# Performance work log

Hardware: AMD Instinct MI355X
Metric: run time of the kernel (lower is better)

The kernel has to match this reference:

```python
import jax, jax.numpy as jnp
import numpy as np

N_NODES = 50000
N_NEIB = 64
D = 256
BATCH = 1024
N_SAMPLES = (25, 10)  # fanout per layer (layer_specs n_sample)


def setup_inputs() -> dict:
    key = jax.random.key(0)
    ks = jax.random.split(key, 12)
    inp = {
        'ids': jax.random.randint(ks[0], (BATCH,), 0, N_NODES),
        'diff_idx': jax.random.randint(ks[1], (N_NODES, N_NEIB), 0, N_NODES),
        'diff_val': jax.random.uniform(ks[2], (N_NODES, N_NEIB), dtype=jnp.float32),
        'feats': jax.random.normal(ks[3], (N_NODES, D), dtype=jnp.float32),
    }
    # two aggregator layers, each: fc_x, fc_neib : D -> D (= output_dim//2)
    for li in range(2):
        inp[f'Wx{li+1}'] = jax.random.normal(ks[4 + 4 * li], (D, D), dtype=jnp.float32) * 0.05
        inp[f'bx{li+1}'] = jnp.zeros((D,), dtype=jnp.float32)
        inp[f'Wn{li+1}'] = jax.random.normal(ks[5 + 4 * li], (D, D), dtype=jnp.float32) * 0.05
        inp[f'bn{li+1}'] = jnp.zeros((D,), dtype=jnp.float32)
    return inp


def _sample(diff_idx, diff_val, ids, n_samples, key):
    # gather candidate neighbor rows, shared random column permutation, take first n_samples
    tmp_idx = diff_idx[ids]            # [n, N_NEIB]
    tmp_val = diff_val[ids]
    perm = jax.random.permutation(key, tmp_idx.shape[1])
    idx = tmp_idx[:, perm][:, :n_samples].reshape(-1)
    val = tmp_val[:, perm][:, :n_samples].reshape(-1)
    return idx, val


def _agg(x, neib, vals, Wx, bx, Wn, bn):
    # weighted-mean neighbor aggregation + self/neib linear combine + relu
    n = x.shape[0]
    d = neib.shape[1]
    neib = neib.reshape(n, -1, d)              # [n, s, d]
    vals = vals.reshape(n, -1)                 # [n, s]
    w = vals / (jnp.sum(vals, axis=1, keepdims=True) + 1e-10)
    m = jnp.einsum('nsd,ns->nd', neib, w)      # weighted mean of neighbors
    return jax.nn.relu(x @ Wx + bx + m @ Wn + bn)


def reference(ids, diff_idx, diff_val, feats,
              Wx1, bx1, Wn1, bn1, Wx2, bx2, Wn2, bn2):
    skey = jax.random.key(42)
    all_feats = [feats[ids]]
    all_vals = []
    cur = ids
    for li, n in enumerate(N_SAMPLES):
        cur, vals = _sample(diff_idx, diff_val, cur, n, jax.random.fold_in(skey, li))
        all_feats.append(feats[cur])
        all_vals.append(vals)
    params = [(Wx1, bx1, Wn1, bn1), (Wx2, bx2, Wn2, bn2)]
    for Wx, bx, Wn, bn in params:
        all_feats = [_agg(all_feats[k], all_feats[k + 1], all_vals[k], Wx, bx, Wn, bn)
                     for k in range(len(all_feats) - 1)]
    assert len(all_feats) == 1
    return all_feats[0]  # [BATCH, D]
```

## Files before the change

### kernel.cpp

```cpp
#include <hip/hip_runtime.h>
#include <stdint.h>
#include <stddef.h>
#include <algorithm>

#define BATCH  1024
#define S1     25
#define S2     10
#define DIM    256
#define NNEIB  64
#define L2ROWS (BATCH * S1)
#define MROWS  (BATCH + BATCH * S1)
#define KTOT   512
#define NFEAT  50000

struct Perm25 { int p[S1]; };
struct Perm10 { int p[S2]; };

typedef __attribute__((ext_vector_type(8))) short short8;
typedef __attribute__((ext_vector_type(4))) float f32x4;

static inline uint32_t rotl_(uint32_t x, int d) { return (x << d) | (x >> (32 - d)); }

static void tf2x32(uint32_t k0, uint32_t k1, uint32_t x0, uint32_t x1,
                   uint32_t* o0, uint32_t* o1) {
  const uint32_t ks0 = k0, ks1 = k1, ks2 = k0 ^ k1 ^ 0x1BD11BDAu;
  static const int R[8] = {13, 15, 26, 6, 17, 29, 16, 24};
  x0 += ks0; x1 += ks1;
  for (int g = 0; g < 5; ++g) {
    const int* rr = R + (g & 1) * 4;
    for (int i = 0; i < 4; i++) { x0 += x1; x1 = rotl_(x1, rr[i]); x1 ^= x0; }
    uint32_t a, b;
    switch (g) {
      default:
      case 0: a = ks1; b = ks2; break;
      case 1: a = ks2; b = ks0; break;
      case 2: a = ks0; b = ks1; break;
      case 3: a = ks1; b = ks2; break;
      case 4: a = ks2; b = ks0; break;
    }
    x0 += a; x1 = x1 + b + (uint32_t)(g + 1);
  }
  *o0 = x0; *o1 = x1;
}

static void compute_perm(uint32_t li, int n, int* out) {
  uint32_t k0, k1, s0, s1;
  tf2x32(0u, 42u, 0u, li, &k0, &k1);
  tf2x32(k0, k1, 0u, 1u, &s0, &s1);
  uint32_t bits[NNEIB];
  for (int i = 0; i < NNEIB; i++) {
    uint32_t a, b;
    tf2x32(s0, s1, 0u, (uint32_t)i, &a, &b);
    bits[i] = a ^ b;
  }
  int idx[NNEIB];
  for (int i = 0; i < NNEIB; i++) idx[i] = i;
  std::stable_sort(idx, idx + NNEIB, [&](int A, int B) { return bits[A] < bits[B]; });
  for (int j = 0; j < n; j++) out[j] = idx[j];
}

__device__ __forceinline__ unsigned short f2bf(float x) {
  union { float f; uint32_t u; } v; v.f = x;
  uint32_t r = (v.u + 0x7FFFu + ((v.u >> 16) & 1u)) >> 16;
  return (unsigned short)r;
}
__device__ __forceinline__ float bfbits2f(uint32_t lo16) {
  union { uint32_t u; float f; } v; v.u = lo16 << 16;
  return v.f;
}
__device__ __forceinline__ void gload16(const unsigned short* g, unsigned short* l) {
  __builtin_amdgcn_global_load_lds(
      (const __attribute__((address_space(1))) unsigned int*)g,
      (__attribute__((address_space(3))) unsigned int*)l, 16, 0, 0);
}


#define PREP_CONVF   12500
#define PREP_CONVW   512
#define PREP_BLOCKS  (PREP_CONVF + 2 * PREP_CONVW + 4)
__global__ __launch_bounds__(256) void prep_k(
    const float* __restrict__ feats, uint32_t* __restrict__ fb,
    const float* __restrict__ Wx1, const float* __restrict__ Wn1,
    unsigned short* __restrict__ Wt1,
    const float* __restrict__ Wx2, const float* __restrict__ Wn2,
    unsigned short* __restrict__ Wt2,
    const int* __restrict__ ids, const int* __restrict__ dix,
    const float* __restrict__ dval, int* __restrict__ idx1,
    float* __restrict__ w1, Perm25 pm) {
  int b = blockIdx.x, t = threadIdx.x;
  if (b < PREP_CONVF) {
    int i = b * 256 + t;
    f32x4 v = *(const f32x4*)&feats[(size_t)i * 4];
    uint2 o;
    o.x = f2bf(v.x) | ((uint32_t)f2bf(v.y) << 16);
    o.y = f2bf(v.z) | ((uint32_t)f2bf(v.w) << 16);
    ((uint2*)fb)[i] = o;
  } else if (b < PREP_CONVF + 2 * PREP_CONVW) {
    int wi = b - PREP_CONVF;
    const float* Wx = (wi < PREP_CONVW) ? Wx1 : Wx2;
    const float* Wn = (wi < PREP_CONVW) ? Wn1 : Wn2;
    unsigned short* Wt = (wi < PREP_CONVW) ? Wt1 : Wt2;
    int idx = (wi % PREP_CONVW) * 256 + t;
    int n = idx >> 9, k = idx & 511;
    float v = (k < DIM) ? Wx[(size_t)k * DIM + n] : Wn[(size_t)(k - DIM) * DIM + n];
    Wt[(size_t)n * KTOT + k] = f2bf(v);
  } else {
    int i = (b - PREP_CONVF - 2 * PREP_CONVW) * 256 + t;
    if (i >= BATCH) return;
    int nid = ids[i];
    const float* vr = dval + (size_t)nid * NNEIB;
    const int* ir = dix + (size_t)nid * NNEIB;
    float v[S1];
    float s = 0.f;
    for (int j = 0; j < S1; j++) { v[j] = vr[pm.p[j]]; s += v[j]; }
    float inv = 1.f / (s + 1e-10f);
    for (int j = 0; j < S1; j++) {
      w1[i * S1 + j] = v[j] * inv;
      idx1[i * S1 + j] = ir[pm.p[j]];
    }
  }
}

__global__ __launch_bounds__(256) void stage1_k(
    const uint2* __restrict__ fb, const int* __restrict__ ids,
    const int* __restrict__ idx1, const float* __restrict__ w1,
    const int* __restrict__ dix, const float* __restrict__ dval, Perm10 pm2,
    uint2* __restrict__ A1) {
  int wave = threadIdx.x >> 6, lane = threadIdx.x & 63;
  int r = blockIdx.x * 4 + wave;
  float a0 = 0.f, a1 = 0.f, a2 = 0.f, a3 = 0.f;
  int xr;
  if (r < BATCH) {
    xr = ids[r];
    int nbl = 0; float wl = 0.f;
    if (lane < S1) { nbl = idx1[r * S1 + lane]; wl = w1[r * S1 + lane]; }
#pragma unroll
    for (int j = 0; j < S1; j++) {
      int nid = __shfl(nbl, j);
      float wj = __shfl(wl, j);
      uint2 u = fb[(size_t)nid * 64 + lane];
      a0 += wj * bfbits2f(u.x & 0xffffu);
      a1 += wj * bfbits2f(u.x >> 16);
      a2 += wj * bfbits2f(u.y & 0xffffu);
      a3 += wj * bfbits2f(u.y >> 16);
    }
  } else {
    int nx = idx1[r - BATCH];
    xr = nx;
    int nbl = 0; float vj = 0.f;
    if (lane < S2) {
      int c = pm2.p[lane];
      nbl = dix[(size_t)nx * NNEIB + c];
      vj = dval[(size_t)nx * NNEIB + c];
    }
    float tot = 0.f;
#pragma unroll
    for (int j = 0; j < S2; j++) tot += __shfl(vj, j);
    float wl = vj / (tot + 1e-10f);
#pragma unroll
    for (int j = 0; j < S2; j++) {
      int nid = __shfl(nbl, j);
      float wj = __shfl(wl, j);
      uint2 u = fb[(size_t)nid * 64 + lane];
      a0 += wj * bfbits2f(u.x & 0xffffu);
      a1 += wj * bfbits2f(u.x >> 16);
      a2 += wj * bfbits2f(u.y & 0xffffu);
      a3 += wj * bfbits2f(u.y >> 16);
    }
  }
  uint2 xv = fb[(size_t)xr * 64 + lane];
  uint2 o;
  o.x = f2bf(a0) | ((uint32_t)f2bf(a1) << 16);
  o.y = f2bf(a2) | ((uint32_t)f2bf(a3) << 16);
  A1[(size_t)r * 128 + lane] = xv;
  A1[(size_t)r * 128 + 64 + lane] = o;
}

__global__ __launch_bounds__(256) void stage2_k(
    const uint2* __restrict__ Hb, const float* __restrict__ w1,
    uint2* __restrict__ A2) {
  int wave = threadIdx.x >> 6, lane = threadIdx.x & 63;
  int i = blockIdx.x * 4 + wave;
  float wl = (lane < S1) ? w1[(size_t)i * S1 + lane] : 0.f;
  const uint2* hb = Hb + (size_t)(BATCH + i * S1) * 64 + lane;
  float a0 = 0.f, a1 = 0.f, a2 = 0.f, a3 = 0.f;
#pragma unroll
  for (int j = 0; j < S1; j++) {
    float wj = __shfl(wl, j);
    uint2 u = hb[(size_t)j * 64];
    a0 += wj * bfbits2f(u.x & 0xffffu);
    a1 += wj * bfbits2f(u.x >> 16);
    a2 += wj * bfbits2f(u.y & 0xffffu);
    a3 += wj * bfbits2f(u.y >> 16);
  }
  uint2 xv = Hb[(size_t)i * 64 + lane];
  uint2 o;
  o.x = f2bf(a0) | ((uint32_t)f2bf(a1) << 16);
  o.y = f2bf(a2) | ((uint32_t)f2bf(a3) << 16);
  A2[(size_t)i * 128 + lane] = xv;
  A2[(size_t)i * 128 + 64 + lane] = o;
}

#define BK 32
template <int TBM, int TBN, bool OUT_BF16>
__global__ __launch_bounds__(256) void gemm_k(
    const unsigned short* __restrict__ A, const unsigned short* __restrict__ Wt,
    const float* __restrict__ bx, const float* __restrict__ bn,
    void* __restrict__ OutP) {
  constexpr int MI = TBM / 32;
  constexpr int NJ = TBN / 32;
  __shared__ __align__(16) unsigned short As[TBM][BK];
  __shared__ __align__(16) unsigned short Bs[TBN][BK];
  int t = threadIdx.x;
  int wave = t >> 6, lane = t & 63, quad = lane >> 4, l16 = lane & 15;
  int wm = (wave >> 1) * (TBM / 2);
  int wn = (wave & 1) * (TBN / 2);
  int row0 = blockIdx.x * TBM, col0 = blockIdx.y * TBN;

  f32x4 acc[MI][NJ];
#pragma unroll
  for (int i = 0; i < MI; i++)
#pragma unroll
    for (int j = 0; j < NJ; j++) acc[i][j] = (f32x4){0.f, 0.f, 0.f, 0.f};

  int rl = lane >> 2;
  int cl = (lane & 3) * 8;

  for (int k0 = 0; k0 < KTOT; k0 += BK) {
#pragma unroll
    for (int c = 0; c < TBM / 64; c++) {
      int row = c * 64 + wave * 16 + rl;
      gload16(A + (size_t)(row0 + row) * KTOT + k0 + cl, &As[c * 64 + wave * 16][0]);
    }
#pragma unroll
    for (int c = 0; c < TBN / 64; c++) {
      int row = c * 64 + wave * 16 + rl;
      gload16(Wt + (size_t)(col0 + row) * KTOT + k0 + cl, &Bs[c * 64 + wave * 16][0]);
    }
    __syncthreads();

    short8 af[MI], bfr[NJ];
#pragma unroll
    for (int i = 0; i < MI; i++)
      af[i] = *(const short8*)&As[wm + i * 16 + l16][quad * 8];
#pragma unroll
    for (int j = 0; j < NJ; j++)
      bfr[j] = *(const short8*)&Bs[wn + j * 16 + l16][quad * 8];
#pragma unroll
    for (int i = 0; i < MI; i++)
#pragma unroll
      for (int j = 0; j < NJ; j++)
        acc[i][j] = __builtin_amdgcn_mfma_f32_16x16x32_bf16(af[i], bfr[j], acc[i][j], 0, 0, 0);
    __syncthreads();
  }

  float bias[NJ];
#pragma unroll
  for (int j = 0; j < NJ; j++) {
    int c = col0 + wn + j * 16 + l16;
    bias[j] = bx[c] + bn[c];
  }
#pragma unroll
  for (int i = 0; i < MI; i++) {
#pragma unroll
    for (int j = 0; j < NJ; j++) {
      int c = col0 + wn + j * 16 + l16;
#pragma unroll
      for (int reg = 0; reg < 4; reg++) {
        int r = row0 + wm + i * 16 + quad * 4 + reg;
        float v = fmaxf(acc[i][j][reg] + bias[j], 0.f);
        if (OUT_BF16)
          ((unsigned short*)OutP)[(size_t)r * DIM + c] = f2bf(v);
        else
          ((float*)OutP)[(size_t)r * DIM + c] = v;
      }
    }
  }
}

static inline size_t align256(size_t x) { return (x + 255) & ~(size_t)255; }

extern "C" void kernel_launch(void* const* d_in, const int* in_sizes, int n_in,
                              void* d_out, int out_size, void* d_ws, size_t ws_size,
                              hipStream_t stream) {
  const int*   ids  = (const int*)d_in[0];
  const int*   dix  = (const int*)d_in[1];
  const float* dval = (const float*)d_in[2];
  const float* feats= (const float*)d_in[3];
  const float* Wx1  = (const float*)d_in[4];
  const float* bx1  = (const float*)d_in[5];
  const float* Wn1  = (const float*)d_in[6];
  const float* bn1  = (const float*)d_in[7];
  const float* Wx2  = (const float*)d_in[8];
  const float* bx2  = (const float*)d_in[9];
  const float* Wn2  = (const float*)d_in[10];
  const float* bn2  = (const float*)d_in[11];
  float* out = (float*)d_out;

  Perm25 p25;
  Perm10 p10;
  compute_perm(0u, S1, p25.p);
  compute_perm(1u, S2, p10.p);

  char* w = (char*)d_ws;
  int*            idx1 = (int*)w;            w += align256(sizeof(int) * L2ROWS);
  float*          w1   = (float*)w;          w += align256(sizeof(float) * L2ROWS);
  uint32_t*       fb   = (uint32_t*)w;       w += align256(2 * (size_t)NFEAT * DIM);
  unsigned short* A1   = (unsigned short*)w; w += align256(2 * (size_t)MROWS * KTOT);
  unsigned short* Hb   = (unsigned short*)w; w += align256(2 * (size_t)MROWS * DIM);
  unsigned short* A2   = (unsigned short*)w; w += align256(2 * (size_t)BATCH * KTOT);
  unsigned short* Wt1  = (unsigned short*)w; w += align256(2 * (size_t)DIM * KTOT);
  unsigned short* Wt2  = (unsigned short*)w; w += align256(2 * (size_t)DIM * KTOT);

  prep_k<<<PREP_BLOCKS, 256, 0, stream>>>(feats, fb, Wx1, Wn1, Wt1, Wx2, Wn2, Wt2,
                                          ids, dix, dval, idx1, w1, p25);
  stage1_k<<<MROWS / 4, 256, 0, stream>>>((const uint2*)fb, ids, idx1, w1, dix, dval,
                                          p10, (uint2*)A1);
  gemm_k<128, 128, true><<<dim3(MROWS / 128, DIM / 128), 256, 0, stream>>>(
      A1, Wt1, bx1, bn1, Hb);
  stage2_k<<<BATCH / 4, 256, 0, stream>>>((const uint2*)Hb, w1, (uint2*)A2);
  gemm_k<64, 64, false><<<dim3(BATCH / 64, DIM / 64), 256, 0, stream>>>(
      A2, Wt2, bx2, bn2, out);
}
```

Baseline: 182.9 us.

## Gather self features directly in GEMM and aggregate neighbor pairs with 16-byte loads

The stage kernels no longer copy self-feature rows into a concatenated A buffer. The GEMM instead gathers x rows straight from the bf16 feature table (via ids/idx1) for the first half of K and reads the separate aggregated-neighbor buffer for the second half. Stage1 also splits each wave into two 32-lane halves that each fetch a full 512-byte row with uint4 loads, handling two neighbors per iteration, then combines the halves with a cross-lane shuffle. This removes a write and reread of the self-feature half and halves the gather loop trip count, at the cost of scattered row reads inside the GEMM A-tile loads.

```diff
diff --git a/kernel.cpp b/kernel.cpp
--- a/kernel.cpp
+++ b/kernel.cpp
@@ -121,32 +121,36 @@
   }
 }
 
+template <int S>
+__device__ __forceinline__ void agg_pairs(const uint4* __restrict__ fb, int nbl,
+                                          float wl, int lane, float a[8]) {
+  int h = lane >> 5, l5 = lane & 31;
+#pragma unroll
+  for (int p = 0; p < (S + 1) / 2; p++) {
+    int jj = 2 * p + h;
+    int nid = __shfl(nbl, (jj < S) ? jj : 0);
+    float wj = (jj < S) ? __shfl(wl, jj) : 0.f;
+    uint4 u = fb[(size_t)nid * 32 + l5];
+    a[0] += wj * bfbits2f(u.x & 0xffffu); a[1] += wj * bfbits2f(u.x >> 16);
+    a[2] += wj * bfbits2f(u.y & 0xffffu); a[3] += wj * bfbits2f(u.y >> 16);
+    a[4] += wj * bfbits2f(u.z & 0xffffu); a[5] += wj * bfbits2f(u.z >> 16);
+    a[6] += wj * bfbits2f(u.w & 0xffffu); a[7] += wj * bfbits2f(u.w >> 16);
+  }
+}
+
 __global__ __launch_bounds__(256) void stage1_k(
-    const uint2* __restrict__ fb, const int* __restrict__ ids,
-    const int* __restrict__ idx1, const float* __restrict__ w1,
-    const int* __restrict__ dix, const float* __restrict__ dval, Perm10 pm2,
-    uint2* __restrict__ A1) {
+    const uint4* __restrict__ fb, const int* __restrict__ idx1,
+    const float* __restrict__ w1, const int* __restrict__ dix,
+    const float* __restrict__ dval, Perm10 pm2, uint4* __restrict__ M1) {
   int wave = threadIdx.x >> 6, lane = threadIdx.x & 63;
   int r = blockIdx.x * 4 + wave;
-  float a0 = 0.f, a1 = 0.f, a2 = 0.f, a3 = 0.f;
-  int xr;
+  float a[8] = {0.f, 0.f, 0.f, 0.f, 0.f, 0.f, 0.f, 0.f};
   if (r < BATCH) {
-    xr = ids[r];
     int nbl = 0; float wl = 0.f;
     if (lane < S1) { nbl = idx1[r * S1 + lane]; wl = w1[r * S1 + lane]; }
-#pragma unroll
-    for (int j = 0; j < S1; j++) {
-      int nid = __shfl(nbl, j);
-      float wj = __shfl(wl, j);
-      uint2 u = fb[(size_t)nid * 64 + lane];
-      a0 += wj * bfbits2f(u.x & 0xffffu);
-      a1 += wj * bfbits2f(u.x >> 16);
-      a2 += wj * bfbits2f(u.y & 0xffffu);
-      a3 += wj * bfbits2f(u.y >> 16);
-    }
+    agg_pairs<S1>(fb, nbl, wl, lane, a);
   } else {
     int nx = idx1[r - BATCH];
-    xr = nx;
     int nbl = 0; float vj = 0.f;
     if (lane < S2) {
       int c = pm2.p[lane];
@@ -157,28 +161,23 @@
 #pragma unroll
     for (int j = 0; j < S2; j++) tot += __shfl(vj, j);
     float wl = vj / (tot + 1e-10f);
-#pragma unroll
-    for (int j = 0; j < S2; j++) {
-      int nid = __shfl(nbl, j);
-      float wj = __shfl(wl, j);
-      uint2 u = fb[(size_t)nid * 64 + lane];
-      a0 += wj * bfbits2f(u.x & 0xffffu);
-      a1 += wj * bfbits2f(u.x >> 16);
-      a2 += wj * bfbits2f(u.y & 0xffffu);
-      a3 += wj * bfbits2f(u.y >> 16);
-    }
-  }
-  uint2 xv = fb[(size_t)xr * 64 + lane];
-  uint2 o;
-  o.x = f2bf(a0) | ((uint32_t)f2bf(a1) << 16);
-  o.y = f2bf(a2) | ((uint32_t)f2bf(a3) << 16);
-  A1[(size_t)r * 128 + lane] = xv;
-  A1[(size_t)r * 128 + 64 + lane] = o;
+    agg_pairs<S2>(fb, nbl, wl, lane, a);
+  }
+#pragma unroll
+  for (int q = 0; q < 8; q++) a[q] += __shfl_xor(a[q], 32);
+  if (lane < 32) {
+    uint4 o;
+    o.x = f2bf(a[0]) | ((uint32_t)f2bf(a[1]) << 16);
+    o.y = f2bf(a[2]) | ((uint32_t)f2bf(a[3]) << 16);
+    o.z = f2bf(a[4]) | ((uint32_t)f2bf(a[5]) << 16);
+    o.w = f2bf(a[6]) | ((uint32_t)f2bf(a[7]) << 16);
+    M1[(size_t)r * 32 + (lane & 31)] = o;
+  }
 }
 
 __global__ __launch_bounds__(256) void stage2_k(
     const uint2* __restrict__ Hb, const float* __restrict__ w1,
-    uint2* __restrict__ A2) {
+    uint2* __restrict__ M2) {
   int wave = threadIdx.x >> 6, lane = threadIdx.x & 63;
   int i = blockIdx.x * 4 + wave;
   float wl = (lane < S1) ? w1[(size_t)i * S1 + lane] : 0.f;
@@ -193,20 +192,19 @@
     a2 += wj * bfbits2f(u.y & 0xffffu);
     a3 += wj * bfbits2f(u.y >> 16);
   }
-  uint2 xv = Hb[(size_t)i * 64 + lane];
   uint2 o;
   o.x = f2bf(a0) | ((uint32_t)f2bf(a1) << 16);
   o.y = f2bf(a2) | ((uint32_t)f2bf(a3) << 16);
-  A2[(size_t)i * 128 + lane] = xv;
-  A2[(size_t)i * 128 + 64 + lane] = o;
+  M2[(size_t)i * 64 + lane] = o;
 }
 
 #define BK 32
-template <int TBM, int TBN, bool OUT_BF16>
+template <int TBM, int TBN, bool OUT_BF16, bool GATHER>
 __global__ __launch_bounds__(256) void gemm_k(
-    const unsigned short* __restrict__ A, const unsigned short* __restrict__ Wt,
-    const float* __restrict__ bx, const float* __restrict__ bn,
-    void* __restrict__ OutP) {
+    const unsigned short* __restrict__ Ax, const int* __restrict__ ids,
+    const int* __restrict__ idx1, const unsigned short* __restrict__ Am,
+    const unsigned short* __restrict__ Wt, const float* __restrict__ bx,
+    const float* __restrict__ bn, void* __restrict__ OutP) {
   constexpr int MI = TBM / 32;
   constexpr int NJ = TBN / 32;
   __shared__ __align__(16) unsigned short As[TBM][BK];
@@ -226,12 +224,20 @@
   int rl = lane >> 2;
   int cl = (lane & 3) * 8;
 
+  const unsigned short* xsrc[TBM / 64];
+  const unsigned short* msrc[TBM / 64];
+#pragma unroll
+  for (int c = 0; c < TBM / 64; c++) {
+    int grow = row0 + c * 64 + wave * 16 + rl;
+    int xr = GATHER ? ((grow < BATCH) ? ids[grow] : idx1[grow - BATCH]) : grow;
+    xsrc[c] = Ax + (size_t)xr * DIM + cl;
+    msrc[c] = Am + (size_t)grow * DIM + cl - DIM;
+  }
+
   for (int k0 = 0; k0 < KTOT; k0 += BK) {
 #pragma unroll
-    for (int c = 0; c < TBM / 64; c++) {
-      int row = c * 64 + wave * 16 + rl;
-      gload16(A + (size_t)(row0 + row) * KTOT + k0 + cl, &As[c * 64 + wave * 16][0]);
-    }
+    for (int c = 0; c < TBM / 64; c++)
+      gload16(((k0 < DIM) ? xsrc[c] : msrc[c]) + k0, &As[c * 64 + wave * 16][0]);
 #pragma unroll
     for (int c = 0; c < TBN / 64; c++) {
       int row = c * 64 + wave * 16 + rl;
@@ -306,19 +312,19 @@
   int*            idx1 = (int*)w;            w += align256(sizeof(int) * L2ROWS);
   float*          w1   = (float*)w;          w += align256(sizeof(float) * L2ROWS);
   uint32_t*       fb   = (uint32_t*)w;       w += align256(2 * (size_t)NFEAT * DIM);
-  unsigned short* A1   = (unsigned short*)w; w += align256(2 * (size_t)MROWS * KTOT);
+  unsigned short* M1   = (unsigned short*)w; w += align256(2 * (size_t)MROWS * DIM);
   unsigned short* Hb   = (unsigned short*)w; w += align256(2 * (size_t)MROWS * DIM);
-  unsigned short* A2   = (unsigned short*)w; w += align256(2 * (size_t)BATCH * KTOT);
+  unsigned short* M2   = (unsigned short*)w; w += align256(2 * (size_t)BATCH * DIM);
   unsigned short* Wt1  = (unsigned short*)w; w += align256(2 * (size_t)DIM * KTOT);
   unsigned short* Wt2  = (unsigned short*)w; w += align256(2 * (size_t)DIM * KTOT);
 
   prep_k<<<PREP_BLOCKS, 256, 0, stream>>>(feats, fb, Wx1, Wn1, Wt1, Wx2, Wn2, Wt2,
                                           ids, dix, dval, idx1, w1, p25);
-  stage1_k<<<MROWS / 4, 256, 0, stream>>>((const uint2*)fb, ids, idx1, w1, dix, dval,
-                                          p10, (uint2*)A1);
-  gemm_k<128, 128, true><<<dim3(MROWS / 128, DIM / 128), 256, 0, stream>>>(
-      A1, Wt1, bx1, bn1, Hb);
-  stage2_k<<<BATCH / 4, 256, 0, stream>>>((const uint2*)Hb, w1, (uint2*)A2);
-  gemm_k<64, 64, false><<<dim3(BATCH / 64, DIM / 64), 256, 0, stream>>>(
-      A2, Wt2, bx2, bn2, out);
-}
+  stage1_k<<<MROWS / 4, 256, 0, stream>>>((const uint4*)fb, idx1, w1, dix, dval, p10,
+                                          (uint4*)M1);
+  gemm_k<128, 128, true, true><<<dim3(MROWS / 128, DIM / 128), 256, 0, stream>>>(
+      (const unsigned short*)fb, ids, idx1, M1, Wt1, bx1, bn1, Hb);
+  stage2_k<<<BATCH / 4, 256, 0, stream>>>((const uint2*)Hb, w1, (uint2*)M2);
+  gemm_k<64, 64, false, false><<<dim3(BATCH / 64, DIM / 64), 256, 0, stream>>>(
+      Hb, nullptr, nullptr, M2, Wt2, bx2, bn2, out);
+}
```

Result: no change. 183.1 us (+0.1%).
